# Optimization experiments

Measured on AMD Instinct MI355X. Metric: run time of the kernel, lower is better.

The kernel has to match this reference:

```python
import jax, jax.numpy as jnp
import numpy as np

B, T, E, D = 8, 2048, 1024, 64  # batch, seq, embed_dim, head_dim

def setup_inputs() -> dict:
    key = jax.random.key(0)
    kx, kq, kk, kv = jax.random.split(key, 4)
    scale = 1.0 / np.sqrt(E)
    return {
        "x": jax.random.normal(kx, (B, T, E), dtype=jnp.float32),
        "Wq": jax.random.normal(kq, (E, D), dtype=jnp.float32) * scale,
        "Wk": jax.random.normal(kk, (E, D), dtype=jnp.float32) * scale,
        "Wv": jax.random.normal(kv, (E, D), dtype=jnp.float32) * scale,
    }

def reference(x, Wq, Wk, Wv):
    # single-head causal attention (dropout in eval mode = identity)
    q = jnp.einsum('bte,ed->btd', x, Wq)
    k = jnp.einsum('bte,ed->btd', x, Wk)
    v = jnp.einsum('bte,ed->btd', x, Wv)
    head_dim = q.shape[-1]
    wei = jnp.einsum('btd,bsd->bts', q, k) * (head_dim ** -0.5)  # [B,T,T]
    causal = jnp.tril(jnp.ones((wei.shape[1], wei.shape[2]), dtype=bool))
    wei = jnp.where(causal, wei, -jnp.inf)
    wei = jax.nn.softmax(wei, axis=-1)
    out = jnp.einsum('bts,bsd->btd', wei, v)  # [B,T,D]
    return out
```

## Files before the change

kernel.cpp:

```cpp
#include <hip/hip_runtime.h>
#include <hip/hip_bf16.h>
#include <cstdint>
#include <cstddef>

#define B_ 8
#define T_ 2048
#define E_ 1024
#define D_ 64

typedef __attribute__((ext_vector_type(8))) short bf16x8;
typedef __attribute__((ext_vector_type(4))) float f32x4;
typedef __attribute__((ext_vector_type(16))) float f32x16;
typedef __attribute__((ext_vector_type(4))) unsigned short u16x4;

#define QSCALE 0.1803368801111204f

__device__ __forceinline__ short f2bf(float f){
    __hip_bfloat16 h = __float2bfloat16(f);
    return *reinterpret_cast<short*>(&h);
}

__device__ __forceinline__ bf16x8 cvt8v(const f32x4 a, const f32x4 b){
    bf16x8 r;
    r[0]=f2bf(a[0]); r[1]=f2bf(a[1]); r[2]=f2bf(a[2]); r[3]=f2bf(a[3]);
    r[4]=f2bf(b[0]); r[5]=f2bf(b[1]); r[6]=f2bf(b[2]); r[7]=f2bf(b[3]);
    return r;
}

__global__ __launch_bounds__(256) void wconv_kernel(
    const float* __restrict__ Wq, const float* __restrict__ Wk,
    const float* __restrict__ Wv, __hip_bfloat16* __restrict__ Wfrag)
{
    const int g = blockIdx.x*256 + threadIdx.x;
    const int l = g & 63;
    const int ntg = (g >> 6) % 6;
    const int cg = g / 384;
    const int n = ntg*32 + (l & 31);
    const int m = n >> 6;
    const int ncol = n & 63;
    const float* W = (m==0) ? Wq : (m==1) ? Wk : Wv;
    const float sc = (m==0) ? QSCALE : 1.0f;
    const int k0 = cg*16 + (l>>5)*8;
    bf16x8 r;
    #pragma unroll
    for (int j=0;j<8;++j)
        r[j] = f2bf(W[(size_t)(k0+j)*64 + ncol] * sc);
    *reinterpret_cast<bf16x8*>(Wfrag + (size_t)g*8) = r;
}

__global__ __launch_bounds__(384, 3) void proj_kernel(
    const float* __restrict__ x, const __hip_bfloat16* __restrict__ Wfrag,
    __hip_bfloat16* __restrict__ Qo, __hip_bfloat16* __restrict__ Ko,
    __hip_bfloat16* __restrict__ VTg)
{
    __shared__ __align__(16) unsigned short xs[2][32*64];
    __shared__ float vt[32*65];
    const int tid = threadIdx.x;
    const int w = tid>>6, l = tid&63;
    const int l31 = l&31, kg = l>>5;
    const float* xp = x + (size_t)blockIdx.x*32*E_;

    f32x16 acc;
    #pragma unroll
    for (int j=0;j<16;++j) acc[j]=0.f;

    const bf16x8* Wfp = reinterpret_cast<const bf16x8*>(Wfrag);

    bf16x8 btA[4], btB[4];
    #pragma unroll
    for (int c=0;c<4;++c)
        btA[c] = Wfp[(size_t)(((0*4+c)*6 + w)*64 + l)];

    const int srow = tid>>3, sc8 = tid&7;

    if (tid < 256){
        f32x4 v0 = *reinterpret_cast<const f32x4*>(xp + (size_t)srow*E_ + sc8*8);
        f32x4 v1 = *reinterpret_cast<const f32x4*>(xp + (size_t)srow*E_ + sc8*8 + 4);
        *reinterpret_cast<bf16x8*>((char*)&xs[0][0] + srow*128 + ((sc8*16) ^ ((srow&7)<<4))) = cvt8v(v0, v1);
    }
    __syncthreads();

#define PSTEP(T, BC, BN)                                                       \
    {                                                                          \
        const int t = (T);                                                     \
        if (t+1 < 16){                                                         \
            _Pragma("unroll")                                                  \
            for (int c=0;c<4;++c)                                              \
                BN[c] = Wfp[(size_t)((((t+1)*4+c)*6 + w)*64 + l)];             \
        }                                                                      \
        f32x4 xa0, xa1;                                                        \
        if (t+1 < 16 && tid < 256){                                            \
            xa0 = *reinterpret_cast<const f32x4*>(xp + (size_t)srow*E_ + (t+1)*64 + sc8*8);     \
            xa1 = *reinterpret_cast<const f32x4*>(xp + (size_t)srow*E_ + (t+1)*64 + sc8*8 + 4); \
        }                                                                      \
        const char* xb = (const char*)&xs[t&1][0];                             \
        _Pragma("unroll")                                                      \
        for (int c=0;c<4;++c){                                                 \
            bf16x8 af = *reinterpret_cast<const bf16x8*>(xb + l31*128 + (((c*32 + kg*16)) ^ ((l31&7)<<4))); \
            acc = __builtin_amdgcn_mfma_f32_32x32x16_bf16(af, BC[c], acc, 0,0,0); \
        }                                                                      \
        if (t+1 < 16){                                                         \
            if (tid < 256)                                                     \
                *reinterpret_cast<bf16x8*>((char*)&xs[(t+1)&1][0] + srow*128 + ((sc8*16) ^ ((srow&7)<<4))) = cvt8v(xa0, xa1); \
            __syncthreads();                                                   \
        }                                                                      \
    }

    for (int t2=0; t2<8; ++t2){
        PSTEP(2*t2,   btA, btB)
        PSTEP(2*t2+1, btB, btA)
    }
#undef PSTEP

    const size_t rowBase = (size_t)blockIdx.x*32;
    const int mat = w>>1;
    const int col = (w&1)*32 + l31;
    if (mat < 2){
        __hip_bfloat16* dst = (mat==0) ? Qo : Ko;
        #pragma unroll
        for (int reg=0; reg<16; ++reg){
            const int mr = (reg&3) + 8*(reg>>2) + 4*kg;
            dst[(rowBase + mr)*64 + col] = __float2bfloat16(acc[reg]);
        }
    }
    if (mat == 2){
        #pragma unroll
        for (int reg=0; reg<16; ++reg){
            const int mr = (reg&3) + 8*(reg>>2) + 4*kg;
            vt[mr*65 + col] = acc[reg];
        }
    }
    __syncthreads();
    if (tid < 256){
        const int bb = blockIdx.x >> 6;
        const int t0 = (blockIdx.x & 63)*32;
        const int d = tid>>2, rseg = tid&3;
        bf16x8 pk;
        #pragma unroll
        for (int j=0;j<8;++j)
            pk[j] = f2bf(vt[(rseg*8+j)*65 + d]);
        *reinterpret_cast<bf16x8*>(VTg + (size_t)bb*64*T_ + (size_t)d*T_ + t0 + rseg*8) = pk;
    }
}

__global__ __launch_bounds__(256) void repack_kernel(
    const __hip_bfloat16* __restrict__ Qb, const __hip_bfloat16* __restrict__ Kb,
    const __hip_bfloat16* __restrict__ VTb,
    __hip_bfloat16* __restrict__ Qfrag, __hip_bfloat16* __restrict__ Kfrag,
    __hip_bfloat16* __restrict__ Vfrag)
{
    const int blk = blockIdx.x;
    const int tid = threadIdx.x;
    if (blk < 512){
        const int g = blk*256 + tid;
        const int l = g & 63, ks = (g>>6)&1, nt = (g>>7)&3, t = (g>>9)&31, b = g>>14;
        const int l15 = l&15, lg = l>>4;
        bf16x8 v = *reinterpret_cast<const bf16x8*>(
            Kb + ((size_t)b*T_ + t*64 + nt*16 + l15)*64 + ks*32 + lg*8);
        *reinterpret_cast<bf16x8*>(Kfrag + (size_t)g*8) = v;
    } else if (blk < 1024){
        const int g = (blk-512)*256 + tid;
        const int l = g & 63, ks = (g>>6)&1, dt = (g>>7)&3, t = (g>>9)&31, b = g>>14;
        const int l15 = l&15, lg = l>>4;
        bf16x8 v = *reinterpret_cast<const bf16x8*>(
            VTb + (size_t)b*64*T_ + (size_t)(dt*16 + l15)*T_ + t*64 + ks*32 + lg*8);
        *reinterpret_cast<bf16x8*>(Vfrag + (size_t)g*8) = v;
    } else {
        const int g = (blk-1024)*256 + tid;
        const int l = g & 63, ks = (g>>6)&1, s = (g>>7)&127, b = g>>14;
        const int l15 = l&15, lg = l>>4;
        bf16x8 v = *reinterpret_cast<const bf16x8*>(
            Qb + ((size_t)b*T_ + s*16 + l15)*64 + ks*32 + lg*8);
        *reinterpret_cast<bf16x8*>(Qfrag + (size_t)g*8) = v;
    }
}

__global__ __launch_bounds__(256, 2) void fattn_kernel(
    const __hip_bfloat16* __restrict__ Qfrag, const __hip_bfloat16* __restrict__ Kfrag,
    const __hip_bfloat16* __restrict__ Vfrag, float* __restrict__ out)
{
    __shared__ __align__(16) unsigned short Pl[4][16*64];
    __shared__ float Morg[4][2][16];
    __shared__ float Lorg[4][2][16];
    __shared__ __align__(16) float Oorg[4][2][16*64];

    const int tid = threadIdx.x;
    const int w = tid>>6, l = tid&63;
    const int l15 = l&15, lg = l>>4;

    const int b = blockIdx.x & 7;
    const int p = blockIdx.x >> 3;
    const int sA = p, sB = 127 - p;
    const int nA = (sA>>2) + 1, nB = (sB>>2) + 1;
    const int NU = nA + nB;
    const size_t batchoff = (size_t)b * T_ * 64;

    const bf16x8* qfp = reinterpret_cast<const bf16x8*>(Qfrag);
    const bf16x8* kfp = reinterpret_cast<const bf16x8*>(Kfrag);
    const bf16x8* vfp = reinterpret_cast<const bf16x8*>(Vfrag);
    char* pw = (char*)&Pl[w][0];

    const int qrA = sA*16 + l15, qrB = sB*16 + l15;
    const bf16x8 qA0 = qfp[(size_t)((b*128 + sA)*2 + 0)*64 + l];
    const bf16x8 qA1 = qfp[(size_t)((b*128 + sA)*2 + 1)*64 + l];
    const bf16x8 qB0 = qfp[(size_t)((b*128 + sB)*2 + 0)*64 + l];
    const bf16x8 qB1 = qfp[(size_t)((b*128 + sB)*2 + 1)*64 + l];

    f32x4 oA[4], oB[4];
    #pragma unroll
    for (int i=0;i<4;++i){ oA[i] = (f32x4){0.f,0.f,0.f,0.f}; oB[i] = (f32x4){0.f,0.f,0.f,0.f}; }
    float mA = -1e30f, lA = 0.f, mB = -1e30f, lB = 0.f;

    bf16x8 kf[8], vf[8];

    {
        const int u0 = w;
        const int kvt = (u0 < nA ? u0 : u0 - nA);
        #pragma unroll
        for (int ks=0;ks<2;++ks)
            #pragma unroll
            for (int nt=0;nt<4;++nt)
                kf[ks*4+nt] = kfp[(size_t)(((b*32 + kvt)*4 + nt)*2 + ks)*64 + l];
    }

    auto body = [&](f32x4 (&o)[4], float &mrun, float &lrun,
                    const bf16x8 &qf0, const bf16x8 &qf1,
                    int qrow, int kv0, bool diag, bool hasN, int kvtn)
    {
        f32x4 s4[4];
        #pragma unroll
        for (int nt=0;nt<4;++nt) s4[nt] = (f32x4){0.f,0.f,0.f,0.f};
        __builtin_amdgcn_s_setprio(1);
        #pragma unroll
        for (int ks=0;ks<2;++ks){
            const bf16x8 qf = ks ? qf1 : qf0;
            #pragma unroll
            for (int nt=0;nt<4;++nt)
                s4[nt] = __builtin_amdgcn_mfma_f32_16x16x32_bf16(kf[ks*4+nt], qf, s4[nt], 0,0,0);
        }
        __builtin_amdgcn_s_setprio(0);

        if (hasN){
            #pragma unroll
            for (int ks=0;ks<2;++ks)
                #pragma unroll
                for (int nt=0;nt<4;++nt)
                    kf[ks*4+nt] = kfp[(size_t)(((b*32 + kvtn)*4 + nt)*2 + ks)*64 + l];
        }

        if (diag){
            #pragma unroll
            for (int nt=0;nt<4;++nt)
                #pragma unroll
                for (int rr=0;rr<4;++rr){
                    const int kv = kv0 + nt*16 + lg*4 + rr;
                    if (kv > qrow) s4[nt][rr] = -1e30f;
                }
        }

        float pm;
        {
            float m0 = fmaxf(fmaxf(s4[0][0],s4[0][1]), fmaxf(s4[0][2],s4[0][3]));
            float m1 = fmaxf(fmaxf(s4[1][0],s4[1][1]), fmaxf(s4[1][2],s4[1][3]));
            float m2 = fmaxf(fmaxf(s4[2][0],s4[2][1]), fmaxf(s4[2][2],s4[2][3]));
            float m3 = fmaxf(fmaxf(s4[3][0],s4[3][1]), fmaxf(s4[3][2],s4[3][3]));
            pm = fmaxf(fmaxf(m0,m1), fmaxf(m2,m3));
        }
        pm = fmaxf(pm, __shfl_xor(pm, 16));
        pm = fmaxf(pm, __shfl_xor(pm, 32));
        if (pm > mrun + 8.0f){
            const float scl = exp2f(mrun - pm);
            mrun = pm; lrun *= scl;
            #pragma unroll
            for (int dt=0;dt<4;++dt)
                #pragma unroll
                for (int j=0;j<4;++j) o[dt][j] *= scl;
        }
        float rs = 0.f;
        #pragma unroll
        for (int nt=0;nt<4;++nt)
            #pragma unroll
            for (int rr=0;rr<4;++rr){
                const float pv = exp2f(s4[nt][rr] - mrun);
                s4[nt][rr] = pv; rs += pv;
            }
        rs += __shfl_xor(rs, 16);
        rs += __shfl_xor(rs, 32);
        lrun += rs;

        #pragma unroll
        for (int nt=0;nt<4;++nt){
            u16x4 pk;
            #pragma unroll
            for (int rr=0;rr<4;++rr) pk[rr] = (unsigned short)f2bf(s4[nt][rr]);
            *reinterpret_cast<u16x4*>(pw + l15*128 + ((nt*32 + lg*8) ^ ((l15&7)<<4))) = pk;
        }

        __builtin_amdgcn_s_setprio(1);
        #pragma unroll
        for (int ks=0;ks<2;++ks){
            bf16x8 pf = *reinterpret_cast<const bf16x8*>(pw + l15*128 + ((ks*64 + lg*16) ^ ((l15&7)<<4)));
            #pragma unroll
            for (int dt=0;dt<4;++dt)
                o[dt] = __builtin_amdgcn_mfma_f32_16x16x32_bf16(vf[ks*4+dt], pf, o[dt], 0,0,0);
        }
        __builtin_amdgcn_s_setprio(0);
    };

    for (int u = w; u < NU; u += 4){
        const bool isA = (u < nA);
        const int kvt = isA ? u : (u - nA);
        const int kv0 = kvt*64;
        const bool diag = isA ? (kvt == nA-1) : (kvt == nB-1);

        #pragma unroll
        for (int ks=0;ks<2;++ks)
            #pragma unroll
            for (int dt=0;dt<4;++dt)
                vf[ks*4+dt] = vfp[(size_t)(((b*32 + kvt)*4 + dt)*2 + ks)*64 + l];

        const int un = u + 4;
        const bool hasN = un < NU;
        const int kvtn = hasN ? (un < nA ? un : un - nA) : 0;

        if (isA) body(oA, mA, lA, qA0, qA1, qrA, kv0, diag, hasN, kvtn);
        else     body(oB, mB, lB, qB0, qB1, qrB, kv0, diag, hasN, kvtn);
    }

    #pragma unroll
    for (int dt=0;dt<4;++dt){
        *reinterpret_cast<f32x4*>(&Oorg[w][0][l15*64 + dt*16 + lg*4]) = oA[dt];
        *reinterpret_cast<f32x4*>(&Oorg[w][1][l15*64 + dt*16 + lg*4]) = oB[dt];
    }
    if (lg == 0){
        Morg[w][0][l15] = mA; Lorg[w][0][l15] = lA;
        Morg[w][1][l15] = mB; Lorg[w][1][l15] = lB;
    }
    __syncthreads();
    {
        const int h = tid>>7, q = (tid>>3)&15, d0 = (tid&7)*8;
        const float m0=Morg[0][h][q], m1=Morg[1][h][q], m2=Morg[2][h][q], m3=Morg[3][h][q];
        const float M = fmaxf(fmaxf(m0,m1), fmaxf(m2,m3));
        const float a0=exp2f(m0-M), a1=exp2f(m1-M), a2=exp2f(m2-M), a3=exp2f(m3-M);
        const float L = a0*Lorg[0][h][q] + a1*Lorg[1][h][q] + a2*Lorg[2][h][q] + a3*Lorg[3][h][q];
        const float inv = 1.0f / L;
        const int s = h ? sB : sA;
        float* op = out + batchoff + (size_t)(s*16 + q)*64 + d0;
        #pragma unroll
        for (int j=0;j<8;++j){
            const float v = a0*Oorg[0][h][q*64+d0+j] + a1*Oorg[1][h][q*64+d0+j]
                          + a2*Oorg[2][h][q*64+d0+j] + a3*Oorg[3][h][q*64+d0+j];
            op[j] = v * inv;
        }
    }
}

extern "C" void kernel_launch(void* const* d_in, const int* in_sizes, int n_in,
                              void* d_out, int out_size, void* d_ws, size_t ws_size,
                              hipStream_t stream) {
    const float* x  = (const float*)d_in[0];
    const float* Wq = (const float*)d_in[1];
    const float* Wk = (const float*)d_in[2];
    const float* Wv = (const float*)d_in[3];
    float* out = (float*)d_out;

    const size_t NTOK = (size_t)B_*T_*64;
    __hip_bfloat16* Wfrag = (__hip_bfloat16*)d_ws;
    __hip_bfloat16* Qb    = Wfrag + (size_t)24576*8;
    __hip_bfloat16* Kb    = Qb + NTOK;
    __hip_bfloat16* VTb   = Kb + NTOK;
    __hip_bfloat16* Qfrag = VTb + NTOK;
    __hip_bfloat16* Kfrag = Qfrag + NTOK;
    __hip_bfloat16* Vfrag = Kfrag + NTOK;

    wconv_kernel<<<96, 256, 0, stream>>>(Wq, Wk, Wv, Wfrag);
    proj_kernel<<<512, 384, 0, stream>>>(x, Wfrag, Qb, Kb, VTb);
    repack_kernel<<<1536, 256, 0, stream>>>(Qb, Kb, VTb, Qfrag, Kfrag, Vfrag);
    fattn_kernel<<<512, 256, 0, stream>>>(Qfrag, Kfrag, Vfrag, out);
}
```

Measured before the change: 44.16 us.

## Fuse fragment repack into projection, widen K phases, defer softmax reductions

The projection kernel now writes Q, K and V straight into the MFMA fragment layouts that attention consumes, so the separate repack kernel and its intermediate round trip through global memory are gone. The projection loop now handles 128 columns of E per phase with two alternating accumulators, which halves the number of barriers and breaks the MFMA dependency chain. In attention, the row-max shuffle now runs only when some lane needs a rescale (checked with __any). The row-sum shuffles are dropped in favour of per-lane partial sums that are combined in the final merge. The cost is more shared-memory staging and barriers in the projection epilogue, plus a larger Lorg buffer.

Result: slower. 47.43 us (+7.4%).

```diff
diff --git a/kernel.cpp b/kernel.cpp
--- a/kernel.cpp
+++ b/kernel.cpp
@@ -50,128 +50,149 @@
 
 __global__ __launch_bounds__(384, 3) void proj_kernel(
     const float* __restrict__ x, const __hip_bfloat16* __restrict__ Wfrag,
-    __hip_bfloat16* __restrict__ Qo, __hip_bfloat16* __restrict__ Ko,
-    __hip_bfloat16* __restrict__ VTg)
+    __hip_bfloat16* __restrict__ Qfrag, __hip_bfloat16* __restrict__ Kfrag,
+    __hip_bfloat16* __restrict__ Vfrag)
 {
-    __shared__ __align__(16) unsigned short xs[2][32*64];
+    __shared__ __align__(16) unsigned short xs[2][32*128];
     __shared__ float vt[32*65];
     const int tid = threadIdx.x;
     const int w = tid>>6, l = tid&63;
     const int l31 = l&31, kg = l>>5;
+    const int l15 = l&15, lg = l>>4;
     const float* xp = x + (size_t)blockIdx.x*32*E_;
 
-    f32x16 acc;
-    #pragma unroll
-    for (int j=0;j<16;++j) acc[j]=0.f;
+    f32x16 accE, accO;
+    #pragma unroll
+    for (int j=0;j<16;++j){ accE[j]=0.f; accO[j]=0.f; }
 
     const bf16x8* Wfp = reinterpret_cast<const bf16x8*>(Wfrag);
 
-    bf16x8 btA[4], btB[4];
-    #pragma unroll
-    for (int c=0;c<4;++c)
-        btA[c] = Wfp[(size_t)(((0*4+c)*6 + w)*64 + l)];
-
-    const int srow = tid>>3, sc8 = tid&7;
+    bf16x8 btA[8], btB[8];
+    #pragma unroll
+    for (int c=0;c<8;++c)
+        btA[c] = Wfp[(size_t)((c*6 + w)*64 + l)];
+
+    const int srow = tid>>4, sg = tid&15;
 
     if (tid < 256){
-        f32x4 v0 = *reinterpret_cast<const f32x4*>(xp + (size_t)srow*E_ + sc8*8);
-        f32x4 v1 = *reinterpret_cast<const f32x4*>(xp + (size_t)srow*E_ + sc8*8 + 4);
-        *reinterpret_cast<bf16x8*>((char*)&xs[0][0] + srow*128 + ((sc8*16) ^ ((srow&7)<<4))) = cvt8v(v0, v1);
-    }
-    __syncthreads();
-
-#define PSTEP(T, BC, BN)                                                       \
+        #pragma unroll
+        for (int pass=0; pass<2; ++pass){
+            const int row = pass*16 + srow;
+            f32x4 v0 = *reinterpret_cast<const f32x4*>(xp + (size_t)row*E_ + sg*8);
+            f32x4 v1 = *reinterpret_cast<const f32x4*>(xp + (size_t)row*E_ + sg*8 + 4);
+            *reinterpret_cast<bf16x8*>((char*)&xs[0][0] + row*256 + ((sg ^ (row&15))<<4)) = cvt8v(v0, v1);
+        }
+    }
+    __syncthreads();
+
+#define PPHASE(P, BC, BN)                                                      \
     {                                                                          \
-        const int t = (T);                                                     \
-        if (t+1 < 16){                                                         \
+        const int p = (P);                                                     \
+        if (p+1 < 8){                                                          \
             _Pragma("unroll")                                                  \
-            for (int c=0;c<4;++c)                                              \
-                BN[c] = Wfp[(size_t)((((t+1)*4+c)*6 + w)*64 + l)];             \
+            for (int c=0;c<8;++c)                                              \
+                BN[c] = Wfp[(size_t)((((p+1)*8+c)*6 + w)*64 + l)];             \
         }                                                                      \
-        f32x4 xa0, xa1;                                                        \
-        if (t+1 < 16 && tid < 256){                                            \
-            xa0 = *reinterpret_cast<const f32x4*>(xp + (size_t)srow*E_ + (t+1)*64 + sc8*8);     \
-            xa1 = *reinterpret_cast<const f32x4*>(xp + (size_t)srow*E_ + (t+1)*64 + sc8*8 + 4); \
+        f32x4 xa0a, xa0b, xa1a, xa1b;                                          \
+        if (p+1 < 8 && tid < 256){                                             \
+            xa0a = *reinterpret_cast<const f32x4*>(xp + (size_t)srow*E_ + (p+1)*128 + sg*8);        \
+            xa0b = *reinterpret_cast<const f32x4*>(xp + (size_t)srow*E_ + (p+1)*128 + sg*8 + 4);    \
+            xa1a = *reinterpret_cast<const f32x4*>(xp + (size_t)(16+srow)*E_ + (p+1)*128 + sg*8);   \
+            xa1b = *reinterpret_cast<const f32x4*>(xp + (size_t)(16+srow)*E_ + (p+1)*128 + sg*8 + 4);\
         }                                                                      \
-        const char* xb = (const char*)&xs[t&1][0];                             \
+        const char* xb = (const char*)&xs[p&1][0];                             \
         _Pragma("unroll")                                                      \
-        for (int c=0;c<4;++c){                                                 \
-            bf16x8 af = *reinterpret_cast<const bf16x8*>(xb + l31*128 + (((c*32 + kg*16)) ^ ((l31&7)<<4))); \
-            acc = __builtin_amdgcn_mfma_f32_32x32x16_bf16(af, BC[c], acc, 0,0,0); \
+        for (int c=0;c<8;++c){                                                 \
+            bf16x8 af = *reinterpret_cast<const bf16x8*>(xb + l31*256 + (((c*2+kg) ^ (l31&15))<<4)); \
+            if (c & 1) accO = __builtin_amdgcn_mfma_f32_32x32x16_bf16(af, BC[c], accO, 0,0,0);       \
+            else       accE = __builtin_amdgcn_mfma_f32_32x32x16_bf16(af, BC[c], accE, 0,0,0);       \
         }                                                                      \
-        if (t+1 < 16){                                                         \
-            if (tid < 256)                                                     \
-                *reinterpret_cast<bf16x8*>((char*)&xs[(t+1)&1][0] + srow*128 + ((sc8*16) ^ ((srow&7)<<4))) = cvt8v(xa0, xa1); \
+        if (p+1 < 8){                                                          \
+            if (tid < 256){                                                    \
+                char* xd = (char*)&xs[(p+1)&1][0];                             \
+                *reinterpret_cast<bf16x8*>(xd + srow*256 + ((sg ^ (srow&15))<<4)) = cvt8v(xa0a, xa0b);          \
+                *reinterpret_cast<bf16x8*>(xd + (16+srow)*256 + ((sg ^ ((16+srow)&15))<<4)) = cvt8v(xa1a, xa1b);\
+            }                                                                  \
             __syncthreads();                                                   \
         }                                                                      \
     }
 
-    for (int t2=0; t2<8; ++t2){
-        PSTEP(2*t2,   btA, btB)
-        PSTEP(2*t2+1, btB, btA)
-    }
-#undef PSTEP
-
-    const size_t rowBase = (size_t)blockIdx.x*32;
-    const int mat = w>>1;
-    const int col = (w&1)*32 + l31;
-    if (mat < 2){
-        __hip_bfloat16* dst = (mat==0) ? Qo : Ko;
+    for (int p2=0; p2<4; ++p2){
+        PPHASE(2*p2,   btA, btB)
+        PPHASE(2*p2+1, btB, btA)
+    }
+#undef PPHASE
+
+    float accv[16];
+    #pragma unroll
+    for (int j=0;j<16;++j) accv[j] = accE[j] + accO[j];
+
+    const int q = blockIdx.x;
+    const int b = q >> 6;
+    const int q63 = q & 63;
+    const int t  = q63 >> 1;
+
+    const int sl = tid;
+    const int su_w = (sl>>7)&1, ks_w = (sl>>6)&1, lw = sl&63;
+    const int lw15 = lw&15, lwg = lw>>4;
+
+    __syncthreads();
+    if (w < 2){
+        const int col = (w&1)*32 + l31;
         #pragma unroll
         for (int reg=0; reg<16; ++reg){
             const int mr = (reg&3) + 8*(reg>>2) + 4*kg;
-            dst[(rowBase + mr)*64 + col] = __float2bfloat16(acc[reg]);
-        }
-    }
-    if (mat == 2){
+            vt[mr*65 + col] = accv[reg];
+        }
+    }
+    __syncthreads();
+    if (sl < 256){
+        f32x4 a0, a1;
+        #pragma unroll
+        for (int j=0;j<4;++j) a0[j] = vt[(su_w*16+lw15)*65 + ks_w*32 + lwg*8 + j];
+        #pragma unroll
+        for (int j=0;j<4;++j) a1[j] = vt[(su_w*16+lw15)*65 + ks_w*32 + lwg*8 + 4 + j];
+        const size_t gi = ((size_t)(b*128 + 2*q63 + su_w)*2 + ks_w)*64 + lw;
+        *reinterpret_cast<bf16x8*>(Qfrag + gi*8) = cvt8v(a0, a1);
+    }
+    __syncthreads();
+    if (w >= 2 && w < 4){
+        const int col = (w&1)*32 + l31;
         #pragma unroll
         for (int reg=0; reg<16; ++reg){
             const int mr = (reg&3) + 8*(reg>>2) + 4*kg;
-            vt[mr*65 + col] = acc[reg];
-        }
-    }
-    __syncthreads();
-    if (tid < 256){
-        const int bb = blockIdx.x >> 6;
-        const int t0 = (blockIdx.x & 63)*32;
-        const int d = tid>>2, rseg = tid&3;
+            vt[mr*65 + col] = accv[reg];
+        }
+    }
+    __syncthreads();
+    if (sl < 256){
+        f32x4 a0, a1;
+        #pragma unroll
+        for (int j=0;j<4;++j) a0[j] = vt[(su_w*16+lw15)*65 + ks_w*32 + lwg*8 + j];
+        #pragma unroll
+        for (int j=0;j<4;++j) a1[j] = vt[(su_w*16+lw15)*65 + ks_w*32 + lwg*8 + 4 + j];
+        const int nt = (q&1)*2 + su_w;
+        const size_t gi = (((size_t)(b*32 + t)*4 + nt)*2 + ks_w)*64 + lw;
+        *reinterpret_cast<bf16x8*>(Kfrag + gi*8) = cvt8v(a0, a1);
+    }
+    __syncthreads();
+    if (w >= 4){
+        const int col = (w&1)*32 + l31;
+        #pragma unroll
+        for (int reg=0; reg<16; ++reg){
+            const int mr = (reg&3) + 8*(reg>>2) + 4*kg;
+            vt[mr*65 + col] = accv[reg];
+        }
+    }
+    __syncthreads();
+    if (sl < 256){
+        const int dt = sl>>6;
         bf16x8 pk;
         #pragma unroll
         for (int j=0;j<8;++j)
-            pk[j] = f2bf(vt[(rseg*8+j)*65 + d]);
-        *reinterpret_cast<bf16x8*>(VTg + (size_t)bb*64*T_ + (size_t)d*T_ + t0 + rseg*8) = pk;
-    }
-}
-
-__global__ __launch_bounds__(256) void repack_kernel(
-    const __hip_bfloat16* __restrict__ Qb, const __hip_bfloat16* __restrict__ Kb,
-    const __hip_bfloat16* __restrict__ VTb,
-    __hip_bfloat16* __restrict__ Qfrag, __hip_bfloat16* __restrict__ Kfrag,
-    __hip_bfloat16* __restrict__ Vfrag)
-{
-    const int blk = blockIdx.x;
-    const int tid = threadIdx.x;
-    if (blk < 512){
-        const int g = blk*256 + tid;
-        const int l = g & 63, ks = (g>>6)&1, nt = (g>>7)&3, t = (g>>9)&31, b = g>>14;
-        const int l15 = l&15, lg = l>>4;
-        bf16x8 v = *reinterpret_cast<const bf16x8*>(
-            Kb + ((size_t)b*T_ + t*64 + nt*16 + l15)*64 + ks*32 + lg*8);
-        *reinterpret_cast<bf16x8*>(Kfrag + (size_t)g*8) = v;
-    } else if (blk < 1024){
-        const int g = (blk-512)*256 + tid;
-        const int l = g & 63, ks = (g>>6)&1, dt = (g>>7)&3, t = (g>>9)&31, b = g>>14;
-        const int l15 = l&15, lg = l>>4;
-        bf16x8 v = *reinterpret_cast<const bf16x8*>(
-            VTb + (size_t)b*64*T_ + (size_t)(dt*16 + l15)*T_ + t*64 + ks*32 + lg*8);
-        *reinterpret_cast<bf16x8*>(Vfrag + (size_t)g*8) = v;
-    } else {
-        const int g = (blk-1024)*256 + tid;
-        const int l = g & 63, ks = (g>>6)&1, s = (g>>7)&127, b = g>>14;
-        const int l15 = l&15, lg = l>>4;
-        bf16x8 v = *reinterpret_cast<const bf16x8*>(
-            Qb + ((size_t)b*T_ + s*16 + l15)*64 + ks*32 + lg*8);
-        *reinterpret_cast<bf16x8*>(Qfrag + (size_t)g*8) = v;
+            pk[j] = f2bf(vt[(lwg*8+j)*65 + dt*16 + lw15]);
+        const size_t gi = (((size_t)(b*32 + t)*4 + dt)*2 + (q&1))*64 + lw;
+        *reinterpret_cast<bf16x8*>(Vfrag + gi*8) = pk;
     }
 }
 
@@ -181,7 +202,7 @@
 {
     __shared__ __align__(16) unsigned short Pl[4][16*64];
     __shared__ float Morg[4][2][16];
-    __shared__ float Lorg[4][2][16];
+    __shared__ float Lorg[4][2][64];
     __shared__ __align__(16) float Oorg[4][2][16*64];
 
     const int tid = threadIdx.x;
@@ -258,19 +279,21 @@
                 }
         }
 
-        float pm;
+        float pmLoc;
         {
             float m0 = fmaxf(fmaxf(s4[0][0],s4[0][1]), fmaxf(s4[0][2],s4[0][3]));
             float m1 = fmaxf(fmaxf(s4[1][0],s4[1][1]), fmaxf(s4[1][2],s4[1][3]));
             float m2 = fmaxf(fmaxf(s4[2][0],s4[2][1]), fmaxf(s4[2][2],s4[2][3]));
             float m3 = fmaxf(fmaxf(s4[3][0],s4[3][1]), fmaxf(s4[3][2],s4[3][3]));
-            pm = fmaxf(fmaxf(m0,m1), fmaxf(m2,m3));
-        }
-        pm = fmaxf(pm, __shfl_xor(pm, 16));
-        pm = fmaxf(pm, __shfl_xor(pm, 32));
-        if (pm > mrun + 8.0f){
-            const float scl = exp2f(mrun - pm);
-            mrun = pm; lrun *= scl;
+            pmLoc = fmaxf(fmaxf(m0,m1), fmaxf(m2,m3));
+        }
+        if (__any(pmLoc > mrun + 8.0f)){
+            float pm = pmLoc;
+            pm = fmaxf(pm, __shfl_xor(pm, 16));
+            pm = fmaxf(pm, __shfl_xor(pm, 32));
+            const float mn = fmaxf(mrun, pm);
+            const float scl = exp2f(mrun - mn);
+            mrun = mn; lrun *= scl;
             #pragma unroll
             for (int dt=0;dt<4;++dt)
                 #pragma unroll
@@ -284,8 +307,6 @@
                 const float pv = exp2f(s4[nt][rr] - mrun);
                 s4[nt][rr] = pv; rs += pv;
             }
-        rs += __shfl_xor(rs, 16);
-        rs += __shfl_xor(rs, 32);
         lrun += rs;
 
         #pragma unroll
@@ -332,9 +353,11 @@
         *reinterpret_cast<f32x4*>(&Oorg[w][0][l15*64 + dt*16 + lg*4]) = oA[dt];
         *reinterpret_cast<f32x4*>(&Oorg[w][1][l15*64 + dt*16 + lg*4]) = oB[dt];
     }
+    Lorg[w][0][l] = lA;
+    Lorg[w][1][l] = lB;
     if (lg == 0){
-        Morg[w][0][l15] = mA; Lorg[w][0][l15] = lA;
-        Morg[w][1][l15] = mB; Lorg[w][1][l15] = lB;
+        Morg[w][0][l15] = mA;
+        Morg[w][1][l15] = mB;
     }
     __syncthreads();
     {
@@ -342,7 +365,12 @@
         const float m0=Morg[0][h][q], m1=Morg[1][h][q], m2=Morg[2][h][q], m3=Morg[3][h][q];
         const float M = fmaxf(fmaxf(m0,m1), fmaxf(m2,m3));
         const float a0=exp2f(m0-M), a1=exp2f(m1-M), a2=exp2f(m2-M), a3=exp2f(m3-M);
-        const float L = a0*Lorg[0][h][q] + a1*Lorg[1][h][q] + a2*Lorg[2][h][q] + a3*Lorg[3][h][q];
+        float L = 0.f;
+        #pragma unroll
+        for (int gg=0; gg<4; ++gg){
+            L += a0*Lorg[0][h][gg*16+q] + a1*Lorg[1][h][gg*16+q]
+               + a2*Lorg[2][h][gg*16+q] + a3*Lorg[3][h][gg*16+q];
+        }
         const float inv = 1.0f / L;
         const int s = h ? sB : sA;
         float* op = out + batchoff + (size_t)(s*16 + q)*64 + d0;
@@ -366,15 +394,11 @@
 
     const size_t NTOK = (size_t)B_*T_*64;
     __hip_bfloat16* Wfrag = (__hip_bfloat16*)d_ws;
-    __hip_bfloat16* Qb    = Wfrag + (size_t)24576*8;
-    __hip_bfloat16* Kb    = Qb + NTOK;
-    __hip_bfloat16* VTb   = Kb + NTOK;
-    __hip_bfloat16* Qfrag = VTb + NTOK;
+    __hip_bfloat16* Qfrag = Wfrag + (size_t)24576*8;
     __hip_bfloat16* Kfrag = Qfrag + NTOK;
     __hip_bfloat16* Vfrag = Kfrag + NTOK;
 
     wconv_kernel<<<96, 256, 0, stream>>>(Wq, Wk, Wv, Wfrag);
-    proj_kernel<<<512, 384, 0, stream>>>(x, Wfrag, Qb, Kb, VTb);
-    repack_kernel<<<1536, 256, 0, stream>>>(Qb, Kb, VTb, Qfrag, Kfrag, Vfrag);
+    proj_kernel<<<512, 384, 0, stream>>>(x, Wfrag, Qfrag, Kfrag, Vfrag);
     fattn_kernel<<<512, 256, 0, stream>>>(Qfrag, Kfrag, Vfrag, out);
 }
```
